# Performance work log

Hardware: AMD Instinct MI355X
Metric: run time of the kernel (lower is better)

Reference implementation:

```python
import jax, jax.numpy as jnp
import numpy as np
import math

B, S, K, H, NH = 4, 1024, 512, 1024, 16
HD = H // NH  # 64


def _split_heads(x):
    # [B, L, H] -> [B, NH, L, HD]
    b, l, _ = x.shape
    return x.reshape(b, l, NH, HD).transpose(0, 2, 1, 3)


def setup_inputs() -> dict:
    key = jax.random.key(0)
    ks = jax.random.split(key, 16)
    scale = 1.0 / math.sqrt(H)
    d = {
        'hidden_states': jax.random.normal(ks[0], (B, S, H), jnp.float32),
        'encoder_hidden_states': jax.random.normal(ks[1], (B, K, H), jnp.float32),
        'attention_mask': jnp.zeros((B, 1, 1, S), jnp.float32),
        'encoder_attention_mask': jnp.zeros((B, 1, 1, K), jnp.float32),
    }
    names = ['q', 'k', 'v', 'kq', 'kk', 'kv']
    for i, n in enumerate(names):
        d[f'W{n}'] = jax.random.normal(ks[2 + i], (H, H), jnp.float32) * scale
        d[f'b{n}'] = jnp.zeros((H,), jnp.float32)
    return d


def reference(hidden_states, encoder_hidden_states, attention_mask, encoder_attention_mask,
              Wq, bq, Wk, bk, Wv, bv, Wkq, bkq, Wkk, bkk, Wkv, bkv):
    inv = 1.0 / math.sqrt(HD)
    # self branch
    q = _split_heads(hidden_states @ Wq + bq)            # [B,NH,S,HD]
    k = _split_heads(hidden_states @ Wk + bk)
    v = _split_heads(hidden_states @ Wv + bv)
    scores = jnp.einsum('bhsd,bhtd->bhst', q, k) * inv + attention_mask
    probs = jax.nn.softmax(scores, axis=-1)              # [B,NH,S,S]
    ctx = jnp.einsum('bhst,bhtd->bhsd', probs, v)
    # knowledge branch
    kq = _split_heads(hidden_states @ Wkq + bkq)          # [B,NH,S,HD]
    kk = _split_heads(encoder_hidden_states @ Wkk + bkk)  # [B,NH,K,HD]
    kv = _split_heads(encoder_hidden_states @ Wkv + bkv)
    kscores = jnp.einsum('bhsd,bhtd->bhst', kq, kk) * inv + encoder_attention_mask
    kprobs = jax.nn.softmax(kscores, axis=-1)            # [B,NH,S,K]
    kctx = jnp.einsum('bhst,bhtd->bhsd', kprobs, kv)
    # merge heads and average branches
    out = (ctx + kctx) * 0.5                             # [B,NH,S,HD]
    out = out.transpose(0, 2, 1, 3).reshape(B, S, H)
    return out
```

## Files before the change

### kernel.cpp

```cpp
#include <hip/hip_runtime.h>

#define BATCH 4
#define SEQ   1024
#define KENC  512
#define HDIM  1024
#define NHEAD 16
#define HD    64
#define LOG2E 1.44269504088896340736f

typedef __attribute__((ext_vector_type(8))) short bf16x8;
typedef __attribute__((ext_vector_type(4))) float f32x4;
typedef __attribute__((ext_vector_type(16))) float f32x16;
typedef __attribute__((ext_vector_type(4))) float f4v;
typedef __attribute__((ext_vector_type(4))) short s4v;

__device__ __forceinline__ short f2bf(float f) {
  unsigned u = __float_as_uint(f);
  u += 0x7fffu + ((u >> 16) & 1u);
  return (short)(u >> 16);
}

__device__ __forceinline__ void gload_lds16(const void* g, void* l) {
  __builtin_amdgcn_global_load_lds(
      (const __attribute__((address_space(1))) void*)g,
      (__attribute__((address_space(3))) void*)l, 16, 0, 0);
}

#define MF(A, B, C) __builtin_amdgcn_mfma_f32_16x16x32_bf16((A), (B), (C), 0, 0, 0)

__global__ __launch_bounds__(256) void cast_bf16(const float* __restrict__ src,
                                                 short* __restrict__ dst, int n4) {
  int i = blockIdx.x * 256 + threadIdx.x;
  if (i >= n4) return;
  f4v v = ((const f4v*)src)[i];
  s4v o;
#pragma unroll
  for (int j = 0; j < 4; ++j) o[j] = f2bf(v[j]);
  ((s4v*)dst)[i] = o;
}

struct WtArgs { const float* W[6]; };

__global__ __launch_bounds__(256) void wt_cast(WtArgs a, short* __restrict__ wt) {
  int j = blockIdx.z;
  const float* W = a.W[j];
  short* dst = wt + (size_t)j * (HDIM * HDIM);
  int cb = blockIdx.x * 32, rb = blockIdx.y * 32;
  __shared__ float t[32][33];
  int tx = threadIdx.x & 31, ty = threadIdx.x >> 5;
#pragma unroll
  for (int rr = 0; rr < 4; ++rr)
    t[ty + rr * 8][tx] = W[(size_t)(rb + ty + rr * 8) * HDIM + cb + tx];
  __syncthreads();
#pragma unroll
  for (int rr = 0; rr < 4; ++rr)
    dst[(size_t)(cb + ty + rr * 8) * HDIM + rb + tx] = f2bf(t[tx][ty + rr * 8]);
}

struct ProjArgs {
  const short* X[6];
  const short* Wt[6];
  const float* bias[6];
  short* out[6];
  int M[6];
  int tshift[6];
  int mode[6];
  float scale[6];
};

__global__ __launch_bounds__(256) void proj_gemm(ProjArgs a) {
  int job = blockIdx.z;
  int M = a.M[job];
  int by = blockIdx.y;
  if (by * 128 >= M) return;
  int bx = blockIdx.x;
  const short* X = a.X[job];
  const short* W = a.Wt[job];

  __shared__ __align__(16) char Lds[65536];

  int tid = threadIdx.x, lane = tid & 63, wave = tid >> 6;
  int wr = wave >> 1, wc = wave & 1;
  int l15 = lane & 15, g4 = lane >> 4;

  f32x4 acc[4][4];
#pragma unroll
  for (int m = 0; m < 4; ++m)
#pragma unroll
    for (int n = 0; n < 4; ++n)
#pragma unroll
      for (int r = 0; r < 4; ++r) acc[m][n][r] = 0.0f;

  int arow = by * 128, brow = bx * 128;
  const int crow = lane >> 2;
  const int sgrp = (lane & 3) ^ ((lane >> 2) & 3) ^ (lane >> 4);
  const int rsw = (lane & 3) ^ (l15 >> 2);

  const char* Xb = (const char*)X;
  const char* Wb = (const char*)W;
  const size_t sac0 = ((size_t)(arow + 32 * wave + crow) * HDIM + sgrp * 8) * 2;
  const size_t sac1 = sac0 + (size_t)16 * HDIM * 2;
  const size_t sbc0 = ((size_t)(brow + 32 * wave + crow) * HDIM + sgrp * 8) * 2;
  const size_t sbc1 = sbc0 + (size_t)16 * HDIM * 2;
  const int ldA0 = wave * 2048, ldA1 = ldA0 + 1024;
  const int ldB0 = 8192 + ldA0, ldB1 = ldB0 + 1024;

  const int aoff = wr * 4096 + l15 * 64 + ((g4 ^ rsw) << 4);
  const int boff = 8192 + wc * 4096 + l15 * 64 + ((g4 ^ rsw) << 4);

#define STG_A(SBO, SKT)                                                  \
  do {                                                                   \
    gload_lds16(Xb + sac0 + (size_t)(SKT) * 64, Lds + (SBO) + ldA0);     \
    gload_lds16(Xb + sac1 + (size_t)(SKT) * 64, Lds + (SBO) + ldA1);     \
  } while (0)
#define STG_B(SBO, SKT)                                                  \
  do {                                                                   \
    gload_lds16(Wb + sbc0 + (size_t)(SKT) * 64, Lds + (SBO) + ldB0);     \
    gload_lds16(Wb + sbc1 + (size_t)(SKT) * 64, Lds + (SBO) + ldB1);     \
  } while (0)

  STG_A(0, 0);     STG_B(0, 0);
  STG_A(16384, 1); STG_B(16384, 1);
  STG_A(32768, 2); STG_B(32768, 2);
  asm volatile("s_waitcnt vmcnt(4)" ::: "memory");
  __builtin_amdgcn_s_barrier();
  asm volatile("" ::: "memory");

  bf16x8 xa0, xa1, xb0, xb1, xb2, xb3;
  bf16x8 ya0, ya1, yb0, yb1, yb2, yb3;

  xa0 = *(const bf16x8*)(Lds + 0 * 1024 + aoff);
  xa1 = *(const bf16x8*)(Lds + 1 * 1024 + aoff);
  xb0 = *(const bf16x8*)(Lds + 0 * 1024 + boff);
  xb1 = *(const bf16x8*)(Lds + 1 * 1024 + boff);
  xb2 = *(const bf16x8*)(Lds + 2 * 1024 + boff);
  xb3 = *(const bf16x8*)(Lds + 3 * 1024 + boff);

#define GSTEP_I(BO, BON, CA0, CA1, CB0, CB1, CB2, CB3, NA0, NA1, NB0, NB1,    \
                NB2, NB3, DO_STG, SBO, SKT, DO_NEXT, VMASM, DO_BAR)           \
  do {                                                                        \
    bf16x8 q2 = *(const bf16x8*)(Lds + (BO) + 2 * 1024 + aoff);               \
    bf16x8 q3 = *(const bf16x8*)(Lds + (BO) + 3 * 1024 + aoff);               \
    if (DO_STG) STG_A(SBO, SKT);                                              \
    __builtin_amdgcn_s_setprio(1);                                            \
    acc[0][0] = MF(CA0, CB0, acc[0][0]);                                      \
    acc[0][1] = MF(CA0, CB1, acc[0][1]);                                      \
    acc[0][2] = MF(CA0, CB2, acc[0][2]);                                      \
    acc[0][3] = MF(CA0, CB3, acc[0][3]);                                      \
    acc[1][0] = MF(CA1, CB0, acc[1][0]);                                      \
    acc[1][1] = MF(CA1, CB1, acc[1][1]);                                      \
    acc[1][2] = MF(CA1, CB2, acc[1][2]);                                      \
    acc[1][3] = MF(CA1, CB3, acc[1][3]);                                      \
    __builtin_amdgcn_s_setprio(0);                                            \
    if (DO_NEXT) {                                                            \
      NA0 = *(const bf16x8*)(Lds + (BON) + 0 * 1024 + aoff);                  \
      NA1 = *(const bf16x8*)(Lds + (BON) + 1 * 1024 + aoff);                  \
      NB0 = *(const bf16x8*)(Lds + (BON) + 0 * 1024 + boff);                  \
      NB1 = *(const bf16x8*)(Lds + (BON) + 1 * 1024 + boff);                  \
      NB2 = *(const bf16x8*)(Lds + (BON) + 2 * 1024 + boff);                  \
      NB3 = *(const bf16x8*)(Lds + (BON) + 3 * 1024 + boff);                  \
    }                                                                         \
    if (DO_STG) STG_B(SBO, SKT);                                              \
    __builtin_amdgcn_s_setprio(1);                                            \
    acc[2][0] = MF(q2, CB0, acc[2][0]);                                       \
    acc[2][1] = MF(q2, CB1, acc[2][1]);                                       \
    acc[2][2] = MF(q2, CB2, acc[2][2]);                                       \
    acc[2][3] = MF(q2, CB3, acc[2][3]);                                       \
    acc[3][0] = MF(q3, CB0, acc[3][0]);                                       \
    acc[3][1] = MF(q3, CB1, acc[3][1]);                                       \
    acc[3][2] = MF(q3, CB2, acc[3][2]);                                       \
    acc[3][3] = MF(q3, CB3, acc[3][3]);                                       \
    __builtin_amdgcn_s_setprio(0);                                            \
    asm volatile(VMASM ::: "memory");                                         \
    if (DO_BAR) {                                                             \
      __builtin_amdgcn_s_barrier();                                           \
      asm volatile("" ::: "memory");                                          \
    }                                                                         \
  } while (0)
#define GSTEP(...) GSTEP_I(__VA_ARGS__)

#define XSET xa0, xa1, xb0, xb1, xb2, xb3
#define YSET ya0, ya1, yb0, yb1, yb2, yb3

#pragma unroll 1
  for (int it = 0; it < 7; ++it) {
    int t0 = it * 4;
    GSTEP(0,     16384, XSET, YSET, 1, 49152, t0 + 3, 1, "s_waitcnt vmcnt(4)", 1);
    GSTEP(16384, 32768, YSET, XSET, 1, 0,     t0 + 4, 1, "s_waitcnt vmcnt(4)", 1);
    GSTEP(32768, 49152, XSET, YSET, 1, 16384, t0 + 5, 1, "s_waitcnt vmcnt(4)", 1);
    GSTEP(49152, 0,     YSET, XSET, 1, 32768, t0 + 6, 1, "s_waitcnt vmcnt(4)", 1);
  }
  GSTEP(0,     16384, XSET, YSET, 1, 49152, 31, 1, "s_waitcnt vmcnt(4)", 1);
  GSTEP(16384, 32768, YSET, XSET, 0, 0, 0,      1, "s_waitcnt vmcnt(0)", 1);
  GSTEP(32768, 49152, XSET, YSET, 0, 0, 0,      1, "s_nop 0", 1);
  GSTEP(49152, 0,     YSET, XSET, 0, 0, 0,      0, "s_nop 0", 0);

#undef GSTEP
#undef GSTEP_I
#undef XSET
#undef YSET
#undef STG_A
#undef STG_B

  const float* bias = a.bias[job];
  short* out = a.out[job];
  int tshift = a.tshift[job], tmask = (1 << tshift) - 1, mode = a.mode[job];
  float scl = a.scale[job];
#pragma unroll
  for (int m = 0; m < 4; ++m) {
    int rowb = arow + wr * 64 + m * 16 + (g4 << 2);
#pragma unroll
    for (int n = 0; n < 4; ++n) {
      int col = brow + wc * 64 + n * 16 + l15;
      float bv = bias[col];
      int head = col >> 6, d = col & 63;
#pragma unroll
      for (int r = 0; r < 4; ++r) {
        int row = rowb + r;
        int bb = row >> tshift, t = row & tmask;
        float val = (acc[m][n][r] + bv) * scl;
        size_t idx;
        if (mode == 0)
          idx = ((((size_t)bb * NHEAD + head) << tshift) + t) * 64 + d;
        else
          idx = ((((size_t)bb * NHEAD + head) * 64 + d) << tshift) + t;
        out[idx] = f2bf(val);
      }
    }
  }
}

__global__ __launch_bounds__(256, 3) void attn32(
    const short* __restrict__ qall, const short* __restrict__ kall,
    const short* __restrict__ vTall, const short* __restrict__ kqall,
    const short* __restrict__ kkall, const short* __restrict__ kvTall,
    const float* __restrict__ amask, const float* __restrict__ emask,
    float* __restrict__ out) {
  __shared__ char KT[2][8192];
  __shared__ char VT[2][8192];
  __shared__ float red[4][32];

  int lid = blockIdx.x;
  int id = (lid & 7) * 64 + (lid >> 3);
  int bh = id >> 3, qb = id & 7;
  int b = bh >> 4, h = bh & 15;
  int lane = threadIdx.x & 63, wave = threadIdx.x >> 6;
  int l31 = lane & 31, hi = lane >> 5, x7 = l31 & 7;
  int qrow0 = qb * 128 + wave * 32;

  bf16x8 qcur[4];
  {
    const short* qp = qall + ((size_t)bh * SEQ + qrow0 + l31) * 64;
#pragma unroll
    for (int i = 0; i < 4; ++i)
      qcur[i] = *(const bf16x8*)(qp + i * 16 + hi * 8);
  }

  const char* kb0 = (const char*)(kall + (size_t)bh * SEQ * 64);
  const char* vb0 = (const char*)(vTall + (size_t)bh * 64 * SEQ);
  const char* kb1 = (const char*)(kkall + (size_t)bh * KENC * 64);
  const char* vb1 = (const char*)(kvTall + (size_t)bh * 64 * KENC);
  const float* mpc = amask + (size_t)b * SEQ;

  auto STAGE = [&](int pb, const char* kb, const char* vb, size_t vrowb, int kt) {
    int t0 = threadIdx.x;
#pragma unroll
    for (int c = 0; c < 2; ++c) {
      int idx = c * 256 + t0;
      int row = idx >> 3, phys = idx & 7;
      int lg = phys ^ (row & 7);
      gload_lds16(kb + ((size_t)(kt * 64 + row)) * 128 + lg * 16,
                  KT[pb] + idx * 16);
      gload_lds16(vb + (size_t)row * vrowb + (size_t)kt * 128 + lg * 16,
                  VT[pb] + idx * 16);
    }
  };

  STAGE(0, kb0, vb0, SEQ * 2, 0);

  f32x16 ctx0, ctx1, c10, c11;
#pragma unroll
  for (int r = 0; r < 16; ++r) { ctx0[r] = 0.f; ctx1[r] = 0.f; c10[r] = 0.f; c11[r] = 0.f; }
  float mr = -1e30f, lr = 0.f;

#pragma unroll 1
  for (int t = 0; t < 24; ++t) {
    int p = t & 1;
    __syncthreads();
    if (t < 23) {
      int tn = t + 1;
      if (tn >= 16) STAGE(p ^ 1, kb1, vb1, KENC * 2, tn - 16);
      else          STAGE(p ^ 1, kb0, vb0, SEQ * 2, tn);
    }
    if (t == 16) {
      if (!hi) red[wave][l31] = lr;
      asm volatile("s_waitcnt lgkmcnt(0)" ::: "memory");
#pragma unroll
      for (int r2 = 0; r2 < 4; ++r2) {
        f4v lv = *(const f4v*)(&red[wave][r2 * 8 + 4 * hi]);
#pragma unroll
        for (int j2 = 0; j2 < 4; ++j2) {
          float li = __builtin_amdgcn_rcpf(lv[j2]);
          int r = r2 * 4 + j2;
          c10[r] = ctx0[r] * li;  ctx0[r] = 0.f;
          c11[r] = ctx1[r] * li;  ctx1[r] = 0.f;
        }
      }
      mr = -1e30f; lr = 0.f;
      const short* kqp = kqall + ((size_t)bh * SEQ + qrow0 + l31) * 64;
#pragma unroll
      for (int i = 0; i < 4; ++i)
        qcur[i] = *(const bf16x8*)(kqp + i * 16 + hi * 8);
      mpc = emask + (size_t)b * KENC;
    }
    int kt = (t >= 16) ? t - 16 : t;
    const char* Kp = KT[p];
    const char* Vp = VT[p];

    f32x16 s0, s1;
#pragma unroll
    for (int r = 0; r < 16; ++r) { s0[r] = 0.f; s1[r] = 0.f; }
    __builtin_amdgcn_s_setprio(1);
#pragma unroll
    for (int i = 0; i < 4; ++i) {
      bf16x8 kf = *(const bf16x8*)(Kp + (l31)*128 + (((2 * i + hi) ^ x7) << 4));
      s0 = __builtin_amdgcn_mfma_f32_32x32x16_bf16(kf, qcur[i], s0, 0, 0, 0);
    }
#pragma unroll
    for (int i = 0; i < 4; ++i) {
      bf16x8 kf = *(const bf16x8*)(Kp + (32 + l31) * 128 + (((2 * i + hi) ^ x7) << 4));
      s1 = __builtin_amdgcn_mfma_f32_32x32x16_bf16(kf, qcur[i], s1, 0, 0, 0);
    }
    __builtin_amdgcn_s_setprio(0);

    const float* mp = mpc + kt * 64;
#pragma unroll
    for (int r2 = 0; r2 < 4; ++r2) {
      f4v ma = *(const f4v*)(mp + r2 * 8 + 4 * hi);
      f4v mb = *(const f4v*)(mp + 32 + r2 * 8 + 4 * hi);
#pragma unroll
      for (int j2 = 0; j2 < 4; ++j2) {
        s0[r2 * 4 + j2] = fmaf(ma[j2], LOG2E, s0[r2 * 4 + j2]);
        s1[r2 * 4 + j2] = fmaf(mb[j2], LOG2E, s1[r2 * 4 + j2]);
      }
    }

    float mx = s0[0];
#pragma unroll
    for (int r = 1; r < 16; ++r) mx = fmaxf(mx, s0[r]);
#pragma unroll
    for (int r = 0; r < 16; ++r) mx = fmaxf(mx, s1[r]);
    mx = fmaxf(mx, __int_as_float(__shfl_xor(__float_as_int(mx), 32)));

    if (!__all(mx <= mr + 12.f)) {
      float mn = fmaxf(mr, mx);
      float scl = __builtin_amdgcn_exp2f(mr - mn);
      mr = mn; lr *= scl;
      if (!hi) red[wave][l31] = scl;
      asm volatile("s_waitcnt lgkmcnt(0)" ::: "memory");
#pragma unroll
      for (int r2 = 0; r2 < 4; ++r2) {
        f4v sv = *(const f4v*)(&red[wave][r2 * 8 + 4 * hi]);
#pragma unroll
        for (int j2 = 0; j2 < 4; ++j2) {
          ctx0[r2 * 4 + j2] *= sv[j2];
          ctx1[r2 * 4 + j2] *= sv[j2];
        }
      }
    }

    float rs = 0.f;
#pragma unroll
    for (int r = 0; r < 16; ++r) { s0[r] = __builtin_amdgcn_exp2f(s0[r] - mr); rs += s0[r]; }
#pragma unroll
    for (int r = 0; r < 16; ++r) { s1[r] = __builtin_amdgcn_exp2f(s1[r] - mr); rs += s1[r]; }
    rs += __int_as_float(__shfl_xor(__float_as_int(rs), 32));
    lr += rs;

#pragma unroll
    for (int s = 0; s < 2; ++s) {
      const f32x16& sv = s ? s1 : s0;
      unsigned W[8];
#pragma unroll
      for (int r2 = 0; r2 < 4; ++r2) {
        asm("v_cvt_pk_bf16_f32 %0, %1, %2"
            : "=v"(W[r2 * 2]) : "v"(sv[r2 * 4 + 0]), "v"(sv[r2 * 4 + 1]));
        asm("v_cvt_pk_bf16_f32 %0, %1, %2"
            : "=v"(W[r2 * 2 + 1]) : "v"(sv[r2 * 4 + 2]), "v"(sv[r2 * 4 + 3]));
      }
#pragma unroll
      for (int jr = 0; jr < 2; ++jr) {
        unsigned sendA = hi ? W[(2 * jr) * 2]     : W[(2 * jr + 1) * 2];
        unsigned sendB = hi ? W[(2 * jr) * 2 + 1] : W[(2 * jr + 1) * 2 + 1];
        unsigned rA = (unsigned)__shfl_xor((int)sendA, 32);
        unsigned rB = (unsigned)__shfl_xor((int)sendB, 32);
        union { unsigned u[4]; bf16x8 v; } pa;
        if (!hi) { pa.u[0] = W[2 * jr * 2]; pa.u[1] = W[2 * jr * 2 + 1];
                   pa.u[2] = rA;            pa.u[3] = rB; }
        else     { pa.u[0] = rA;            pa.u[1] = rB;
                   pa.u[2] = W[(2 * jr + 1) * 2]; pa.u[3] = W[(2 * jr + 1) * 2 + 1]; }
        int j = s * 2 + jr;
        __builtin_amdgcn_s_setprio(1);
        bf16x8 vf0 = *(const bf16x8*)(Vp + (l31)*128 + (((2 * j + hi) ^ x7) << 4));
        ctx0 = __builtin_amdgcn_mfma_f32_32x32x16_bf16(pa.v, vf0, ctx0, 0, 0, 0);
        bf16x8 vf1 = *(const bf16x8*)(Vp + (32 + l31) * 128 + (((2 * j + hi) ^ x7) << 4));
        ctx1 = __builtin_amdgcn_mfma_f32_32x32x16_bf16(pa.v, vf1, ctx1, 0, 0, 0);
        __builtin_amdgcn_s_setprio(0);
      }
    }
  }

  if (!hi) red[wave][l31] = lr;
  asm volatile("s_waitcnt lgkmcnt(0)" ::: "memory");
  float* op = out + ((size_t)b * SEQ) * HDIM + h * 64 + l31;
#pragma unroll
  for (int r2 = 0; r2 < 4; ++r2) {
    f4v lv = *(const f4v*)(&red[wave][r2 * 8 + 4 * hi]);
#pragma unroll
    for (int j2 = 0; j2 < 4; ++j2) {
      float li = __builtin_amdgcn_rcpf(lv[j2]);
      int s = qrow0 + r2 * 8 + 4 * hi + j2;
      int r = r2 * 4 + j2;
      op[(size_t)s * HDIM]      = 0.5f * (c10[r] + ctx0[r] * li);
      op[(size_t)s * HDIM + 32] = 0.5f * (c11[r] + ctx1[r] * li);
    }
  }
}

extern "C" void kernel_launch(void* const* d_in, const int* in_sizes, int n_in,
                              void* d_out, int out_size, void* d_ws, size_t ws_size,
                              hipStream_t stream) {
  const float* hid = (const float*)d_in[0];
  const float* enc = (const float*)d_in[1];
  const float* amask = (const float*)d_in[2];
  const float* emask = (const float*)d_in[3];

  char* ws = (char*)d_ws;
  short* hbf = (short*)(ws);
  short* ebf = (short*)(ws + (8u << 20));
  short* wt = (short*)(ws + (12u << 20));
  short* qo = (short*)(ws + (24u << 20));
  short* ko = (short*)(ws + (32u << 20));
  short* vT = (short*)(ws + (40u << 20));
  short* kqo = (short*)(ws + (48u << 20));
  short* kko = (short*)(ws + (56u << 20));
  short* kvT = (short*)(ws + (60u << 20));

  cast_bf16<<<4096, 256, 0, stream>>>(hid, hbf, (BATCH * SEQ * HDIM) / 4);
  cast_bf16<<<2048, 256, 0, stream>>>(enc, ebf, (BATCH * KENC * HDIM) / 4);

  WtArgs wa;
  for (int j = 0; j < 6; ++j) wa.W[j] = (const float*)d_in[4 + 2 * j];
  wt_cast<<<dim3(32, 32, 6), 256, 0, stream>>>(wa, wt);

  ProjArgs pa;
  const short* Xs[6] = {hbf, hbf, hbf, hbf, ebf, ebf};
  short* outs[6] = {qo, ko, vT, kqo, kko, kvT};
  const int Ms[6] = {4096, 4096, 4096, 4096, 2048, 2048};
  const int tsh[6] = {10, 10, 10, 10, 9, 9};
  const int md[6] = {0, 0, 1, 0, 0, 1};
  const float qscale = 0.125f * LOG2E;
  const float scl[6] = {qscale, 1.f, 1.f, qscale, 1.f, 1.f};
  for (int j = 0; j < 6; ++j) {
    pa.X[j] = Xs[j];
    pa.Wt[j] = wt + (size_t)j * (HDIM * HDIM);
    pa.bias[j] = (const float*)d_in[5 + 2 * j];
    pa.out[j] = outs[j];
    pa.M[j] = Ms[j];
    pa.tshift[j] = tsh[j];
    pa.mode[j] = md[j];
    pa.scale[j] = scl[j];
  }
  proj_gemm<<<dim3(8, 32, 6), 256, 0, stream>>>(pa);

  attn32<<<512, 256, 0, stream>>>(qo, ko, vT, kqo, kko, kvT, amask, emask,
                                  (float*)d_out);
}
```

Before: 146.6 us.

## Restructure projection GEMM pipeline, compact grid with XCD remap, merge cast kernels

Replaces the register double-buffered GEMM main loop with a simpler per-step structure. Each step loads fragments from LDS right before its MFMAs and uses explicit barriers, lgkmcnt waits and sched_barriers, with deeper vmcnt waits for a three-stage global-to-LDS prefetch. The 3D grid, which had idle blocks for the shorter encoder jobs, becomes a dense 1D grid of 1280 blocks with an interleaved mapping across the 8 chiplets. The two input cast launches are merged into one kernel. The extra barriers and the loss of register prefetch may expose LDS latency in exchange for fewer idle blocks and one fewer launch.

```diff
diff --git a/kernel.cpp b/kernel.cpp
--- a/kernel.cpp
+++ b/kernel.cpp
@@ -28,15 +28,21 @@
 
 #define MF(A, B, C) __builtin_amdgcn_mfma_f32_16x16x32_bf16((A), (B), (C), 0, 0, 0)
 
-__global__ __launch_bounds__(256) void cast_bf16(const float* __restrict__ src,
-                                                 short* __restrict__ dst, int n4) {
+__global__ __launch_bounds__(256) void cast2(const float* __restrict__ sa,
+                                             short* __restrict__ da, int n4a,
+                                             const float* __restrict__ sb,
+                                             short* __restrict__ db, int n4b) {
   int i = blockIdx.x * 256 + threadIdx.x;
-  if (i >= n4) return;
-  f4v v = ((const f4v*)src)[i];
+  const float* s;
+  short* d;
+  int j;
+  if (i < n4a) { s = sa; d = da; j = i; }
+  else { j = i - n4a; if (j >= n4b) return; s = sb; d = db; }
+  f4v v = ((const f4v*)s)[j];
   s4v o;
 #pragma unroll
-  for (int j = 0; j < 4; ++j) o[j] = f2bf(v[j]);
-  ((s4v*)dst)[i] = o;
+  for (int k = 0; k < 4; ++k) o[k] = f2bf(v[k]);
+  ((s4v*)d)[j] = o;
 }
 
 struct WtArgs { const float* W[6]; };
@@ -62,18 +68,18 @@
   const short* Wt[6];
   const float* bias[6];
   short* out[6];
-  int M[6];
   int tshift[6];
   int mode[6];
   float scale[6];
 };
 
 __global__ __launch_bounds__(256) void proj_gemm(ProjArgs a) {
-  int job = blockIdx.z;
-  int M = a.M[job];
-  int by = blockIdx.y;
-  if (by * 128 >= M) return;
-  int bx = blockIdx.x;
+  int lid = blockIdx.x;
+  int t = (lid & 7) * 160 + (lid >> 3);
+  int job, bx, by;
+  if (t < 1024) { job = t >> 8; int r = t & 255; bx = r & 7; by = r >> 3; }
+  else { int u = t - 1024; job = 4 + (u >> 7); int r = u & 127; bx = r & 7; by = r >> 3; }
+
   const short* X = a.X[job];
   const short* W = a.Wt[job];
 
@@ -122,83 +128,73 @@
   STG_A(0, 0);     STG_B(0, 0);
   STG_A(16384, 1); STG_B(16384, 1);
   STG_A(32768, 2); STG_B(32768, 2);
-  asm volatile("s_waitcnt vmcnt(4)" ::: "memory");
+  asm volatile("s_waitcnt vmcnt(8)" ::: "memory");
   __builtin_amdgcn_s_barrier();
   asm volatile("" ::: "memory");
 
-  bf16x8 xa0, xa1, xb0, xb1, xb2, xb3;
-  bf16x8 ya0, ya1, yb0, yb1, yb2, yb3;
-
-  xa0 = *(const bf16x8*)(Lds + 0 * 1024 + aoff);
-  xa1 = *(const bf16x8*)(Lds + 1 * 1024 + aoff);
-  xb0 = *(const bf16x8*)(Lds + 0 * 1024 + boff);
-  xb1 = *(const bf16x8*)(Lds + 1 * 1024 + boff);
-  xb2 = *(const bf16x8*)(Lds + 2 * 1024 + boff);
-  xb3 = *(const bf16x8*)(Lds + 3 * 1024 + boff);
-
-#define GSTEP_I(BO, BON, CA0, CA1, CB0, CB1, CB2, CB3, NA0, NA1, NB0, NB1,    \
-                NB2, NB3, DO_STG, SBO, SKT, DO_NEXT, VMASM, DO_BAR)           \
+#define STEP(BO, DO_STG, SBO, SKT, VMW, ENDBAR)                               \
   do {                                                                        \
-    bf16x8 q2 = *(const bf16x8*)(Lds + (BO) + 2 * 1024 + aoff);               \
-    bf16x8 q3 = *(const bf16x8*)(Lds + (BO) + 3 * 1024 + aoff);               \
+                   \
+    bf16x8 a0 = *(const bf16x8*)(Lds + (BO) + 0 * 1024 + aoff);               \
+    bf16x8 a1 = *(const bf16x8*)(Lds + (BO) + 1 * 1024 + aoff);               \
+    bf16x8 b0 = *(const bf16x8*)(Lds + (BO) + 0 * 1024 + boff);               \
+    bf16x8 b1 = *(const bf16x8*)(Lds + (BO) + 1 * 1024 + boff);               \
+    bf16x8 b2 = *(const bf16x8*)(Lds + (BO) + 2 * 1024 + boff);               \
+    bf16x8 b3 = *(const bf16x8*)(Lds + (BO) + 3 * 1024 + boff);               \
     if (DO_STG) STG_A(SBO, SKT);                                              \
+    __builtin_amdgcn_sched_barrier(0);                                        \
+    __builtin_amdgcn_s_barrier();                                             \
+    asm volatile("s_waitcnt lgkmcnt(0)" ::: "memory");                        \
+    __builtin_amdgcn_sched_barrier(0);                                        \
     __builtin_amdgcn_s_setprio(1);                                            \
-    acc[0][0] = MF(CA0, CB0, acc[0][0]);                                      \
-    acc[0][1] = MF(CA0, CB1, acc[0][1]);                                      \
-    acc[0][2] = MF(CA0, CB2, acc[0][2]);                                      \
-    acc[0][3] = MF(CA0, CB3, acc[0][3]);                                      \
-    acc[1][0] = MF(CA1, CB0, acc[1][0]);                                      \
-    acc[1][1] = MF(CA1, CB1, acc[1][1]);                                      \
-    acc[1][2] = MF(CA1, CB2, acc[1][2]);                                      \
-    acc[1][3] = MF(CA1, CB3, acc[1][3]);                                      \
+    acc[0][0] = MF(a0, b0, acc[0][0]);                                        \
+    acc[0][1] = MF(a0, b1, acc[0][1]);                                        \
+    acc[0][2] = MF(a0, b2, acc[0][2]);                                        \
+    acc[0][3] = MF(a0, b3, acc[0][3]);                                        \
+    acc[1][0] = MF(a1, b0, acc[1][0]);                                        \
+    acc[1][1] = MF(a1, b1, acc[1][1]);                                        \
+    acc[1][2] = MF(a1, b2, acc[1][2]);                                        \
+    acc[1][3] = MF(a1, b3, acc[1][3]);                                        \
     __builtin_amdgcn_s_setprio(0);                                            \
-    if (DO_NEXT) {                                                            \
-      NA0 = *(const bf16x8*)(Lds + (BON) + 0 * 1024 + aoff);                  \
-      NA1 = *(const bf16x8*)(Lds + (BON) + 1 * 1024 + aoff);                  \
-      NB0 = *(const bf16x8*)(Lds + (BON) + 0 * 1024 + boff);                  \
-      NB1 = *(const bf16x8*)(Lds + (BON) + 1 * 1024 + boff);                  \
-      NB2 = *(const bf16x8*)(Lds + (BON) + 2 * 1024 + boff);                  \
-      NB3 = *(const bf16x8*)(Lds + (BON) + 3 * 1024 + boff);                  \
-    }                                                                         \
+    __builtin_amdgcn_sched_barrier(0);                                        \
+    __builtin_amdgcn_s_barrier();                                             \
+                    \
+    bf16x8 a2 = *(const bf16x8*)(Lds + (BO) + 2 * 1024 + aoff);               \
+    bf16x8 a3 = *(const bf16x8*)(Lds + (BO) + 3 * 1024 + aoff);               \
     if (DO_STG) STG_B(SBO, SKT);                                              \
+    __builtin_amdgcn_sched_barrier(0);                                        \
+    __builtin_amdgcn_s_barrier();                                             \
+    asm volatile("s_waitcnt lgkmcnt(0)" ::: "memory");                        \
+    __builtin_amdgcn_sched_barrier(0);                                        \
     __builtin_amdgcn_s_setprio(1);                                            \
-    acc[2][0] = MF(q2, CB0, acc[2][0]);                                       \
-    acc[2][1] = MF(q2, CB1, acc[2][1]);                                       \
-    acc[2][2] = MF(q2, CB2, acc[2][2]);                                       \
-    acc[2][3] = MF(q2, CB3, acc[2][3]);                                       \
-    acc[3][0] = MF(q3, CB0, acc[3][0]);                                       \
-    acc[3][1] = MF(q3, CB1, acc[3][1]);                                       \
-    acc[3][2] = MF(q3, CB2, acc[3][2]);                                       \
-    acc[3][3] = MF(q3, CB3, acc[3][3]);                                       \
+    acc[2][0] = MF(a2, b0, acc[2][0]);                                        \
+    acc[2][1] = MF(a2, b1, acc[2][1]);                                        \
+    acc[2][2] = MF(a2, b2, acc[2][2]);                                        \
+    acc[2][3] = MF(a2, b3, acc[2][3]);                                        \
+    acc[3][0] = MF(a3, b0, acc[3][0]);                                        \
+    acc[3][1] = MF(a3, b1, acc[3][1]);                                        \
+    acc[3][2] = MF(a3, b2, acc[3][2]);                                        \
+    acc[3][3] = MF(a3, b3, acc[3][3]);                                        \
     __builtin_amdgcn_s_setprio(0);                                            \
-    asm volatile(VMASM ::: "memory");                                         \
-    if (DO_BAR) {                                                             \
+    asm volatile(VMW ::: "memory");                                           \
+    __builtin_amdgcn_sched_barrier(0);                                        \
+    if (ENDBAR) {                                                             \
       __builtin_amdgcn_s_barrier();                                           \
       asm volatile("" ::: "memory");                                          \
     }                                                                         \
   } while (0)
-#define GSTEP(...) GSTEP_I(__VA_ARGS__)
-
-#define XSET xa0, xa1, xb0, xb1, xb2, xb3
-#define YSET ya0, ya1, yb0, yb1, yb2, yb3
 
 #pragma unroll 1
-  for (int it = 0; it < 7; ++it) {
-    int t0 = it * 4;
-    GSTEP(0,     16384, XSET, YSET, 1, 49152, t0 + 3, 1, "s_waitcnt vmcnt(4)", 1);
-    GSTEP(16384, 32768, YSET, XSET, 1, 0,     t0 + 4, 1, "s_waitcnt vmcnt(4)", 1);
-    GSTEP(32768, 49152, XSET, YSET, 1, 16384, t0 + 5, 1, "s_waitcnt vmcnt(4)", 1);
-    GSTEP(49152, 0,     YSET, XSET, 1, 32768, t0 + 6, 1, "s_waitcnt vmcnt(4)", 1);
-  }
-  GSTEP(0,     16384, XSET, YSET, 1, 49152, 31, 1, "s_waitcnt vmcnt(4)", 1);
-  GSTEP(16384, 32768, YSET, XSET, 0, 0, 0,      1, "s_waitcnt vmcnt(0)", 1);
-  GSTEP(32768, 49152, XSET, YSET, 0, 0, 0,      1, "s_nop 0", 1);
-  GSTEP(49152, 0,     YSET, XSET, 0, 0, 0,      0, "s_nop 0", 0);
-
-#undef GSTEP
-#undef GSTEP_I
-#undef XSET
-#undef YSET
+  for (int tt = 0; tt < 29; ++tt) {
+    int bo = (tt & 3) << 14;
+    int sbo = ((tt + 3) & 3) << 14;
+    STEP(bo, 1, sbo, tt + 3, "s_waitcnt vmcnt(8)", 1);
+  }
+  STEP((29 & 3) << 14, 0, 0, 0, "s_waitcnt vmcnt(4)", 1);
+  STEP((30 & 3) << 14, 0, 0, 0, "s_waitcnt vmcnt(0)", 1);
+  STEP((31 & 3) << 14, 0, 0, 0, "s_nop 0", 0);
+
+#undef STEP
 #undef STG_A
 #undef STG_B
 
@@ -217,13 +213,13 @@
 #pragma unroll
       for (int r = 0; r < 4; ++r) {
         int row = rowb + r;
-        int bb = row >> tshift, t = row & tmask;
+        int bb = row >> tshift, tk = row & tmask;
         float val = (acc[m][n][r] + bv) * scl;
         size_t idx;
         if (mode == 0)
-          idx = ((((size_t)bb * NHEAD + head) << tshift) + t) * 64 + d;
+          idx = ((((size_t)bb * NHEAD + head) << tshift) + tk) * 64 + d;
         else
-          idx = ((((size_t)bb * NHEAD + head) * 64 + d) << tshift) + t;
+          idx = ((((size_t)bb * NHEAD + head) * 64 + d) << tshift) + tk;
         out[idx] = f2bf(val);
       }
     }
@@ -446,8 +442,8 @@
   short* kko = (short*)(ws + (56u << 20));
   short* kvT = (short*)(ws + (60u << 20));
 
-  cast_bf16<<<4096, 256, 0, stream>>>(hid, hbf, (BATCH * SEQ * HDIM) / 4);
-  cast_bf16<<<2048, 256, 0, stream>>>(enc, ebf, (BATCH * KENC * HDIM) / 4);
+  cast2<<<6144, 256, 0, stream>>>(hid, hbf, (BATCH * SEQ * HDIM) / 4,
+                                  enc, ebf, (BATCH * KENC * HDIM) / 4);
 
   WtArgs wa;
   for (int j = 0; j < 6; ++j) wa.W[j] = (const float*)d_in[4 + 2 * j];
@@ -456,7 +452,6 @@
   ProjArgs pa;
   const short* Xs[6] = {hbf, hbf, hbf, hbf, ebf, ebf};
   short* outs[6] = {qo, ko, vT, kqo, kko, kvT};
-  const int Ms[6] = {4096, 4096, 4096, 4096, 2048, 2048};
   const int tsh[6] = {10, 10, 10, 10, 9, 9};
   const int md[6] = {0, 0, 1, 0, 0, 1};
   const float qscale = 0.125f * LOG2E;
@@ -466,12 +461,11 @@
     pa.Wt[j] = wt + (size_t)j * (HDIM * HDIM);
     pa.bias[j] = (const float*)d_in[5 + 2 * j];
     pa.out[j] = outs[j];
-    pa.M[j] = Ms[j];
     pa.tshift[j] = tsh[j];
     pa.mode[j] = md[j];
     pa.scale[j] = scl[j];
   }
-  proj_gemm<<<dim3(8, 32, 6), 256, 0, stream>>>(pa);
+  proj_gemm<<<1280, 256, 0, stream>>>(pa);
 
   attn32<<<512, 256, 0, stream>>>(qo, ko, vT, kqo, kko, kvT, amask, emask,
                                   (float*)d_out);
```

After: 151.1 us. 1.03x slower.
